# Optimization experiments

Measured on AMD Instinct MI355X. Metric: run time of the kernel, lower is better.

Reference implementation:

```python
import jax, jax.numpy as jnp
import numpy as np


def setup_inputs() -> dict:
    key = jax.random.key(0)
    k_h, k_src, k_dst, k_w = jax.random.split(key, 4)
    N, F, E, OUT = 100000, 128, 640000, 16
    h = jax.random.normal(k_h, (N, F), dtype=jnp.float32)
    src = jax.random.randint(k_src, (E,), 0, N, dtype=jnp.int64)
    dst = jax.random.randint(k_dst, (E,), 0, N, dtype=jnp.int64)
    # Linear(2F, OUT): weight [OUT, 2F], bias [OUT]
    W = jax.random.normal(k_w, (OUT, 2 * F), dtype=jnp.float32) / np.sqrt(2.0 * F)
    b = jnp.zeros((OUT,), dtype=jnp.float32)
    return {"h": h, "src": src, "dst": dst, "W": W, "b": b}


def reference(h, src, dst, W, b):
    # Per-edge gather of source/dest node features, concat, linear.
    # Dropout is identity in eval mode (p=0.2 during training only).
    h_u = h[src]                      # [E, F]
    h_v = h[dst]                      # [E, F]
    F_dim = h.shape[1]
    W_u, W_v = W[:, :F_dim], W[:, F_dim:]
    # Equivalent to concat([h_u, h_v], -1) @ W.T + b, without materializing concat
    score = jnp.einsum('ef,of->eo', h_u, W_u) + jnp.einsum('ef,of->eo', h_v, W_v) + b
    return score
```

## Files before the change

### kernel.cpp

```cpp
#include <hip/hip_runtime.h>
#include <hip/hip_bf16.h>

#define F_DIM 128
#define OUT_DIM 16

typedef _Float16 half8 __attribute__((ext_vector_type(8)));
typedef float floatx4 __attribute__((ext_vector_type(4)));

__global__ __launch_bounds__(256) void wprep_kernel(
    const float* __restrict__ W, _Float16* __restrict__ Bhi,
    _Float16* __restrict__ Blo)
{
    int tid = blockIdx.x * 256 + threadIdx.x;
    if (tid >= 4096) return;
    int j    = tid & 7;
    int lane = (tid >> 3) & 63;
    int t    = (tid >> 9) & 1;
    int s    = (tid >> 10) & 3;
    int n = lane & 15;
    int q = lane >> 4;
    int k = s * 32 + q * 8 + j;
    float w = W[n * 256 + t * 128 + k];
    _Float16 hi = (_Float16)w;
    _Float16 lo = (_Float16)(w - (float)hi);
    Bhi[tid] = hi;
    Blo[tid] = lo;
}

__global__ __launch_bounds__(256) void proj_mfma_kernel(
    const float* __restrict__ h, const _Float16* __restrict__ Bhi,
    const _Float16* __restrict__ Blo, const float* __restrict__ b,
    float* __restrict__ P, int N)
{
    const int lane = threadIdx.x & 63;
    const int wave = threadIdx.x >> 6;
    const int n = lane & 15;
    const int q = lane >> 4;
    const int row_base = blockIdx.x * 64 + wave * 16;
    if (row_base >= N) return;

    int arow = row_base + n;
    if (arow >= N) arow = N - 1;
    const float* hrow = h + (size_t)arow * F_DIM + q * 8;

    floatx4 c0 = {0.f, 0.f, 0.f, 0.f};
    floatx4 c1 = {0.f, 0.f, 0.f, 0.f};

    #pragma unroll
    for (int s = 0; s < 4; ++s) {
        float av[8];
        *(float4*)(av)     = *(const float4*)(hrow + s * 32);
        *(float4*)(av + 4) = *(const float4*)(hrow + s * 32 + 4);
        half8 ah, al;
        #pragma unroll
        for (int j = 0; j < 8; ++j) {
            _Float16 hi = (_Float16)av[j];
            ah[j] = hi;
            al[j] = (_Float16)(av[j] - (float)hi);
        }
        const int base0 = (s * 2 + 0) * 512 + lane * 8;
        const int base1 = (s * 2 + 1) * 512 + lane * 8;
        half8 bh0 = *(const half8*)(Bhi + base0);
        half8 bl0 = *(const half8*)(Blo + base0);
        half8 bh1 = *(const half8*)(Bhi + base1);
        half8 bl1 = *(const half8*)(Blo + base1);

        c0 = __builtin_amdgcn_mfma_f32_16x16x32_f16(ah, bh0, c0, 0, 0, 0);
        c0 = __builtin_amdgcn_mfma_f32_16x16x32_f16(ah, bl0, c0, 0, 0, 0);
        c0 = __builtin_amdgcn_mfma_f32_16x16x32_f16(al, bh0, c0, 0, 0, 0);
        c1 = __builtin_amdgcn_mfma_f32_16x16x32_f16(ah, bh1, c1, 0, 0, 0);
        c1 = __builtin_amdgcn_mfma_f32_16x16x32_f16(ah, bl1, c1, 0, 0, 0);
        c1 = __builtin_amdgcn_mfma_f32_16x16x32_f16(al, bh1, c1, 0, 0, 0);
    }

    const float bn = b[n];
    #pragma unroll
    for (int reg = 0; reg < 4; ++reg) {
        int row = row_base + q * 4 + reg;
        if (row < N) {
            P[(size_t)row * 32 + n]      = c0[reg] + bn;
            P[(size_t)row * 32 + 16 + n] = c1[reg];
        }
    }
}

__global__ __launch_bounds__(256) void gather_kernel(
    const float* __restrict__ P, const int* __restrict__ src,
    const int* __restrict__ dst, float* __restrict__ out, int E)
{
    const int tid = blockIdx.x * blockDim.x + threadIdx.x;
    const int e = tid >> 2;
    const int q = tid & 3;
    if (e >= E) return;
    const int s = src[e];
    const int d = dst[e];
    const floatx4 pu = *(const floatx4*)(P + (size_t)s * 32 + q * 4);
    const floatx4 pv = *(const floatx4*)(P + (size_t)d * 32 + 16 + q * 4);
    const floatx4 r = pu + pv;
    __builtin_nontemporal_store(r, (floatx4*)out + tid);
}

__global__ __launch_bounds__(256) void direct_kernel(
    const float* __restrict__ h, const int* __restrict__ src,
    const int* __restrict__ dst, const float* __restrict__ W,
    const float* __restrict__ b, float* __restrict__ out, int E)
{
    const int tid = blockIdx.x * blockDim.x + threadIdx.x;
    if (tid >= E * OUT_DIM) return;
    const int e = tid >> 4;
    const int o = tid & 15;
    const float* hu = h + (size_t)src[e] * F_DIM;
    const float* hv = h + (size_t)dst[e] * F_DIM;
    const float* wu = W + (size_t)o * 256;
    const float* wv = wu + 128;
    float acc = b[o];
    for (int k = 0; k < 128; ++k) acc = fmaf(hu[k], wu[k], acc);
    for (int k = 0; k < 128; ++k) acc = fmaf(hv[k], wv[k], acc);
    out[tid] = acc;
}

extern "C" void kernel_launch(void* const* d_in, const int* in_sizes, int n_in,
                              void* d_out, int out_size, void* d_ws, size_t ws_size,
                              hipStream_t stream) {
    const float* h   = (const float*)d_in[0];
    const int*   src = (const int*)d_in[1];
    const int*   dst = (const int*)d_in[2];
    const float* W   = (const float*)d_in[3];
    const float* b   = (const float*)d_in[4];
    float* out = (float*)d_out;

    const int N = in_sizes[0] / F_DIM;
    const int E = in_sizes[1];

    const size_t p_bytes  = (size_t)N * 32 * sizeof(float);
    const size_t p_al     = (p_bytes + 255) & ~(size_t)255;
    const size_t bf_bytes = 4096 * sizeof(_Float16);

    if (ws_size >= p_al + 2 * bf_bytes) {
        float*    P   = (float*)d_ws;
        _Float16* Bhi = (_Float16*)((char*)d_ws + p_al);
        _Float16* Blo = Bhi + 4096;

        wprep_kernel<<<16, 256, 0, stream>>>(W, Bhi, Blo);

        const int blocks1 = (N + 63) / 64;
        proj_mfma_kernel<<<blocks1, 256, 0, stream>>>(h, Bhi, Blo, b, P, N);

        const int total2  = E * 4;
        const int blocks2 = (total2 + 255) / 256;
        gather_kernel<<<blocks2, 256, 0, stream>>>(P, src, dst, out, E);
    } else {
        const int total  = E * OUT_DIM;
        const int blocks = (total + 255) / 256;
        direct_kernel<<<blocks, 256, 0, stream>>>(h, src, dst, W, b, out, E);
    }
}
```

Baseline: 131.7 us.

## Store per-node projections as bf16 in separate u/v tables for gather

The projection kernel now writes the u and v halves into two separate fp32 tables. A new pack kernel rounds both tables to bf16 with round-to-nearest-even, and the gather kernel reads 16-byte bf16 rows from each table instead of 64-byte fp32 rows. This halves the random-gather traffic and makes each gathered row more cache friendly. The cost is an extra kernel launch plus an extra pass over the projections, and a loss of precision: per-edge scores now carry bf16 rounding error, which may exceed the accuracy tolerance.

```diff
diff --git a/kernel.cpp b/kernel.cpp
--- a/kernel.cpp
+++ b/kernel.cpp
@@ -6,6 +6,7 @@
 
 typedef _Float16 half8 __attribute__((ext_vector_type(8)));
 typedef float floatx4 __attribute__((ext_vector_type(4)));
+typedef unsigned short us8 __attribute__((ext_vector_type(8)));
 
 __global__ __launch_bounds__(256) void wprep_kernel(
     const float* __restrict__ W, _Float16* __restrict__ Bhi,
@@ -30,7 +31,7 @@
 __global__ __launch_bounds__(256) void proj_mfma_kernel(
     const float* __restrict__ h, const _Float16* __restrict__ Bhi,
     const _Float16* __restrict__ Blo, const float* __restrict__ b,
-    float* __restrict__ P, int N)
+    float* __restrict__ PuF, float* __restrict__ PvF, int N)
 {
     const int lane = threadIdx.x & 63;
     const int wave = threadIdx.x >> 6;
@@ -78,26 +79,59 @@
     for (int reg = 0; reg < 4; ++reg) {
         int row = row_base + q * 4 + reg;
         if (row < N) {
-            P[(size_t)row * 32 + n]      = c0[reg] + bn;
-            P[(size_t)row * 32 + 16 + n] = c1[reg];
+            PuF[(size_t)row * 16 + n] = c0[reg] + bn;
+            PvF[(size_t)row * 16 + n] = c1[reg];
         }
     }
 }
 
+__device__ __forceinline__ unsigned bf16_bits_rne(float f) {
+    unsigned u = __builtin_bit_cast(unsigned, f);
+    unsigned rounding = 0x7FFFu + ((u >> 16) & 1u);
+    return (u + rounding) >> 16;
+}
+
+__global__ __launch_bounds__(256) void pack_kernel(
+    const float* __restrict__ PuF, const float* __restrict__ PvF,
+    unsigned int* __restrict__ Pu16, unsigned int* __restrict__ Pv16,
+    int total_dwords)
+{
+    int tid = blockIdx.x * 256 + threadIdx.x;
+    if (tid >= 2 * total_dwords) return;
+    const int isV = tid >= total_dwords;
+    const int t = isV ? tid - total_dwords : tid;
+    const float* S = isV ? PvF : PuF;
+    unsigned lo = bf16_bits_rne(S[(size_t)t * 2]);
+    unsigned hi = bf16_bits_rne(S[(size_t)t * 2 + 1]);
+    unsigned packed = lo | (hi << 16);
+    if (isV) Pv16[t] = packed;
+    else     Pu16[t] = packed;
+}
+
 __global__ __launch_bounds__(256) void gather_kernel(
-    const float* __restrict__ P, const int* __restrict__ src,
-    const int* __restrict__ dst, float* __restrict__ out, int E)
+    const unsigned short* __restrict__ Pu, const unsigned short* __restrict__ Pv,
+    const int* __restrict__ src, const int* __restrict__ dst,
+    float* __restrict__ out, int E)
 {
     const int tid = blockIdx.x * blockDim.x + threadIdx.x;
-    const int e = tid >> 2;
-    const int q = tid & 3;
+    const int e = tid >> 1;
+    const int q = tid & 1;
     if (e >= E) return;
     const int s = src[e];
     const int d = dst[e];
-    const floatx4 pu = *(const floatx4*)(P + (size_t)s * 32 + q * 4);
-    const floatx4 pv = *(const floatx4*)(P + (size_t)d * 32 + 16 + q * 4);
-    const floatx4 r = pu + pv;
-    __builtin_nontemporal_store(r, (floatx4*)out + tid);
+    const us8 pu = *(const us8*)(Pu + (size_t)s * 16 + q * 8);
+    const us8 pv = *(const us8*)(Pv + (size_t)d * 16 + q * 8);
+    floatx4 r0, r1;
+    #pragma unroll
+    for (int j = 0; j < 4; ++j) {
+        r0[j] = __uint_as_float((unsigned)pu[j] << 16)
+              + __uint_as_float((unsigned)pv[j] << 16);
+        r1[j] = __uint_as_float((unsigned)pu[j + 4] << 16)
+              + __uint_as_float((unsigned)pv[j + 4] << 16);
+    }
+    floatx4* o = (floatx4*)out + (size_t)tid * 2;
+    __builtin_nontemporal_store(r0, o);
+    __builtin_nontemporal_store(r1, o + 1);
 }
 
 __global__ __launch_bounds__(256) void direct_kernel(
@@ -132,23 +166,34 @@
     const int N = in_sizes[0] / F_DIM;
     const int E = in_sizes[1];
 
-    const size_t p_bytes  = (size_t)N * 32 * sizeof(float);
-    const size_t p_al     = (p_bytes + 255) & ~(size_t)255;
-    const size_t bf_bytes = 4096 * sizeof(_Float16);
-
-    if (ws_size >= p_al + 2 * bf_bytes) {
-        float*    P   = (float*)d_ws;
-        _Float16* Bhi = (_Float16*)((char*)d_ws + p_al);
-        _Float16* Blo = Bhi + 4096;
+    const size_t pf_bytes  = (size_t)N * 16 * sizeof(float);
+    const size_t pf_al     = (pf_bytes + 255) & ~(size_t)255;
+    const size_t p16_bytes = (size_t)N * 8 * sizeof(unsigned);
+    const size_t p16_al    = (p16_bytes + 255) & ~(size_t)255;
+    const size_t bf_bytes  = 4096 * sizeof(_Float16);
+
+    if (ws_size >= 2 * pf_al + 2 * p16_al + 2 * bf_bytes) {
+        float*        PuF  = (float*)d_ws;
+        float*        PvF  = (float*)((char*)d_ws + pf_al);
+        unsigned int* Pu16 = (unsigned int*)((char*)d_ws + 2 * pf_al);
+        unsigned int* Pv16 = (unsigned int*)((char*)d_ws + 2 * pf_al + p16_al);
+        _Float16*     Bhi  = (_Float16*)((char*)d_ws + 2 * pf_al + 2 * p16_al);
+        _Float16*     Blo  = Bhi + 4096;
 
         wprep_kernel<<<16, 256, 0, stream>>>(W, Bhi, Blo);
 
         const int blocks1 = (N + 63) / 64;
-        proj_mfma_kernel<<<blocks1, 256, 0, stream>>>(h, Bhi, Blo, b, P, N);
-
-        const int total2  = E * 4;
+        proj_mfma_kernel<<<blocks1, 256, 0, stream>>>(h, Bhi, Blo, b, PuF, PvF, N);
+
+        const int total_dw = N * 8;
+        const int blocksP  = (2 * total_dw + 255) / 256;
+        pack_kernel<<<blocksP, 256, 0, stream>>>(PuF, PvF, Pu16, Pv16, total_dw);
+
+        const int total2  = E * 2;
         const int blocks2 = (total2 + 255) / 256;
-        gather_kernel<<<blocks2, 256, 0, stream>>>(P, src, dst, out, E);
+        gather_kernel<<<blocks2, 256, 0, stream>>>(
+            (const unsigned short*)Pu16, (const unsigned short*)Pv16,
+            src, dst, out, E);
     } else {
         const int total  = E * OUT_DIM;
         const int blocks = (total + 255) / 256;
```

After: 132.5 us. Within noise of the previous version (+0.7%).
